# Kernel optimization log

Measured on AMD Instinct MI355X. Metric: run time of the kernel, lower is better.

## Reference

```python
import jax, jax.numpy as jnp
import numpy as np

N_NODES = 100000
N_EDGES = 1600000
D_IN, D_HID, D_OUT = 64, 64, 32


def _glorot(key, shape):
    fan_in, fan_out = shape[0], shape[1]
    lim = np.sqrt(6.0 / (fan_in + fan_out)).astype(np.float32)
    return jax.random.uniform(key, shape, jnp.float32, -lim, lim)


def setup_inputs() -> dict:
    key = jax.random.key(0)
    ks = jax.random.split(key, 12)
    x = jax.random.normal(ks[0], (N_NODES, D_IN), jnp.float32)
    edge_index = jax.random.randint(ks[1], (2, N_EDGES), 0, N_NODES, jnp.int64)
    return {
        "x": x,
        "edge_index": edge_index,
        # SAGEConv 1 (in->hid): lin_l (aggregated neighbors, with bias), lin_r (root, no bias)
        "Wl1": _glorot(ks[2], (D_IN, D_HID)),
        "Wr1": _glorot(ks[3], (D_IN, D_HID)),
        "b1": jnp.zeros((D_HID,), jnp.float32),
        # SAGEConv 2 (hid->out)
        "Wl2": _glorot(ks[4], (D_HID, D_OUT)),
        "Wr2": _glorot(ks[5], (D_HID, D_OUT)),
        "b2": jnp.zeros((D_OUT,), jnp.float32),
        # trust head: Linear(32,16) -> ReLU -> Linear(16,1) -> Sigmoid (dropout inert in eval)
        "Wt1": _glorot(ks[6], (D_OUT, 16)),
        "bt1": jnp.zeros((16,), jnp.float32),
        "Wt2": _glorot(ks[7], (16, 1)),
        "bt2": jnp.zeros((1,), jnp.float32),
    }


def _sage_conv(x, src, dst, Wl, Wr, b):
    # mean-aggregate neighbor messages: msg flows src -> dst
    msg = x[src]                                              # [E, d] gather
    agg_sum = jax.ops.segment_sum(msg, dst, num_segments=N_NODES)
    deg = jax.ops.segment_sum(jnp.ones((src.shape[0],), x.dtype), dst,
                              num_segments=N_NODES)
    agg = agg_sum / jnp.maximum(deg, 1.0)[:, None]            # zero-degree -> 0
    return agg @ Wl + x @ Wr + b


def reference(x, edge_index, Wl1, Wr1, b1, Wl2, Wr2, b2, Wt1, bt1, Wt2, bt2):
    src, dst = edge_index[0], edge_index[1]
    h = _sage_conv(x, src, dst, Wl1, Wr1, b1)
    h = jax.nn.relu(h)                    # dropout p=0.3 inert in eval
    h = _sage_conv(h, src, dst, Wl2, Wr2, b2)
    t = jax.nn.relu(h @ Wt1 + bt1)        # dropout p=0.2 inert in eval
    trust = jax.nn.sigmoid(t @ Wt2 + bt2)
    return h, trust
```

## Files before the change

kernel.cpp:

```cpp
#include <hip/hip_runtime.h>
#include <math.h>


#define NBUCK   1563
#define BCAP    1536
#define BKCHUNK 16384
#define RT      16

typedef __attribute__((ext_vector_type(8))) __bf16 bf16x8;
typedef __attribute__((ext_vector_type(4))) float  f32x4;

union BU { bf16x8 v; unsigned short u[8]; };

__device__ inline unsigned short f2bf(float x) {
    unsigned u = __float_as_uint(x);
    unsigned r = u + 0x7fffu + ((u >> 16) & 1u);
    return (unsigned short)(r >> 16);
}
__device__ inline unsigned pack2(float a, float b) {
    return (unsigned)f2bf(a) | ((unsigned)f2bf(b) << 16);
}
__device__ inline float bflo(unsigned u) { return __uint_as_float(u << 16); }
__device__ inline float bfhi(unsigned u) { return __uint_as_float(u & 0xffff0000u); }
__device__ inline float bf2f(unsigned short h) { return __uint_as_float((unsigned)h << 16); }
__device__ inline unsigned packhl(float x) {
    unsigned short h = f2bf(x);
    unsigned short l = f2bf(x - bf2f(h));
    return (unsigned)h | ((unsigned)l << 16);
}

__global__ __launch_bounds__(256) void k_w(
    const float* __restrict__ Wl1, const float* __restrict__ Wr1,
    const float* __restrict__ Wl2, const float* __restrict__ Wr2,
    unsigned short* __restrict__ Wf)
{
    int tid = threadIdx.x;
    for (int idx = tid; idx < 1536; idx += 256) {
        unsigned short hi8[8], lo8[8];
        int base;
        if (idx < 1024) {
            int q = idx >> 6;
            int l = idx & 63;
            int pass = q >> 3, nf = (q >> 1) & 3, kf = q & 1;
            const float* W = pass ? Wr1 : Wl1;
            int col  = nf * 16 + (l & 15);
            int krow = kf * 32 + (l >> 4) * 8;
            #pragma unroll
            for (int e = 0; e < 8; ++e) {
                float w = W[(krow + e) * 64 + col];
                unsigned short h = f2bf(w);
                hi8[e] = h;
                lo8[e] = f2bf(w - bf2f(h));
            }
            base = (q * 2) * 512 + l * 8;
        } else {
            int i2 = idx - 1024;
            int q2 = i2 >> 6;
            int l = i2 & 63;
            int ntile = q2 >> 1, kf = q2 & 1;
            int col  = ntile * 16 + (l & 15);
            const float* W = (col < 32) ? Wl2 : Wr2;
            int c = col & 31;
            int krow = kf * 32 + (l >> 4) * 8;
            #pragma unroll
            for (int e = 0; e < 8; ++e) {
                float w = W[(krow + e) * 32 + c];
                unsigned short h = f2bf(w);
                hi8[e] = h;
                lo8[e] = f2bf(w - bf2f(h));
            }
            base = (32 + q2 * 2) * 512 + l * 8;
        }
        #pragma unroll
        for (int e = 0; e < 8; ++e) {
            Wf[base + e]       = hi8[e];
            Wf[base + 512 + e] = lo8[e];
        }
    }
}

__global__ __launch_bounds__(256) void k_m1(
    const float* __restrict__ x,
    const unsigned short* __restrict__ Wf, const float* __restrict__ b1,
    unsigned* __restrict__ u16b, float* __restrict__ v,
    const int* __restrict__ src, const int* __restrict__ dst,
    int* __restrict__ gcnt, unsigned* __restrict__ pairs,
    int N, int E, int GB, int BKB)
{
    __shared__ int hist[NBUCK];
    int tid = threadIdx.x;
    int g = blockIdx.x / (RT + 1), r = blockIdx.x % (RT + 1);

    if (r == RT) {
        if (g >= BKB) return;
        int e0 = g * BKCHUNK;
        int e1 = min(e0 + BKCHUNK, E);

        for (int i = tid; i < NBUCK; i += 256) hist[i] = 0;
        __syncthreads();
        for (int e = e0 + tid; e < e1; e += 256)
            atomicAdd(&hist[((unsigned)dst[e]) >> 6], 1);
        __syncthreads();
        int cnt[7], base[7];
        #pragma unroll
        for (int t = 0; t < 7; ++t) {
            int i = tid + t * 256;
            cnt[t] = (i < NBUCK) ? hist[i] : 0;
        }
        #pragma unroll
        for (int t = 0; t < 7; ++t) {
            int i = tid + t * 256;
            base[t] = (i < NBUCK) ? atomicAdd(&gcnt[i], cnt[t]) : 0;
        }
        #pragma unroll
        for (int t = 0; t < 7; ++t) {
            int i = tid + t * 256;
            if (i < NBUCK) hist[i] = i * BCAP + base[t];
        }
        __syncthreads();
        for (int e = e0 + tid; e < e1; e += 256) {
            int t = dst[e];
            int b = ((unsigned)t) >> 6;
            int pos = atomicAdd(&hist[b], 1);
            if (pos < (b + 1) * BCAP)
                pairs[pos] = (unsigned)src[e] | ((unsigned)(t & 63) << 17);
        }
        return;
    }

    int tile = RT * g + r;
    if (tile >= GB) return;
    int nblk = tile * 64;

    int l  = tid & 63, wv = tid >> 6;
    int la = l & 15,   g4 = l >> 4;
    int arow = nblk + wv * 16 + la;
    bool rowOK = (arow < N);

    BU ahi[2], alo[2];
    #pragma unroll
    for (int kf = 0; kf < 2; ++kf) {
        float xv[8];
        if (rowOK) {
            const float* xp = &x[(size_t)arow * 64 + kf * 32 + g4 * 8];
            float4 p0 = *(const float4*)xp;
            float4 p1 = *(const float4*)(xp + 4);
            xv[0] = p0.x; xv[1] = p0.y; xv[2] = p0.z; xv[3] = p0.w;
            xv[4] = p1.x; xv[5] = p1.y; xv[6] = p1.z; xv[7] = p1.w;
        } else {
            #pragma unroll
            for (int e = 0; e < 8; ++e) xv[e] = 0.0f;
        }
        #pragma unroll
        for (int e = 0; e < 8; ++e) {
            unsigned short h = f2bf(xv[e]);
            ahi[kf].u[e] = h;
            alo[kf].u[e] = f2bf(xv[e] - bf2f(h));
        }
    }

    unsigned short* u16 = (unsigned short*)u16b;

    #pragma unroll
    for (int pass = 0; pass < 2; ++pass) {
        #pragma unroll
        for (int nf = 0; nf < 4; ++nf) {
            int n0 = nf * 16;
            f32x4 acc = {0.f, 0.f, 0.f, 0.f};
            #pragma unroll
            for (int kf = 0; kf < 2; ++kf) {
                int q2 = ((pass * 4 + nf) * 2 + kf) * 2;
                bf16x8 bhi = *(const bf16x8*)&Wf[(q2 + 0) * 512 + l * 8];
                bf16x8 blo = *(const bf16x8*)&Wf[(q2 + 1) * 512 + l * 8];
                acc = __builtin_amdgcn_mfma_f32_16x16x32_bf16(ahi[kf].v, bhi, acc, 0, 0, 0);
                acc = __builtin_amdgcn_mfma_f32_16x16x32_bf16(alo[kf].v, bhi, acc, 0, 0, 0);
                acc = __builtin_amdgcn_mfma_f32_16x16x32_bf16(ahi[kf].v, blo, acc, 0, 0, 0);
            }
            if (pass == 0) {
                #pragma unroll
                for (int rr = 0; rr < 4; ++rr) {
                    int nd = nblk + wv * 16 + g4 * 4 + rr;
                    if (nd < N)
                        u16[(size_t)nd * 64 + n0 + la] = f2bf(acc[rr]);
                }
            } else {
                float bb = b1[n0 + la];
                #pragma unroll
                for (int rr = 0; rr < 4; ++rr) {
                    int nd = nblk + wv * 16 + g4 * 4 + rr;
                    if (nd < N)
                        v[(size_t)nd * 64 + n0 + la] = acc[rr] + bb;
                }
            }
        }
    }
}

__global__ __launch_bounds__(512) void k_m2(
    const unsigned* __restrict__ pairs, const int* __restrict__ gcnt,
    const unsigned* __restrict__ u16b, const float* __restrict__ v,
    const unsigned short* __restrict__ Wf, const float* __restrict__ b2,
    unsigned* __restrict__ P16b, float* __restrict__ Qout,
    int2* __restrict__ nodeOff, int* __restrict__ adjG, int N)
{
    __shared__ unsigned sHu[64 * 76];
    __shared__ int   sAdj[BCAP];
    __shared__ int   sOff[65];
    __shared__ int   sCur[64];
    int tid = threadIdx.x;
    int b = blockIdx.x;
    int nodeBase = b * 64;
    int base = b * BCAP;
    int count = min(gcnt[b], BCAP);
    const unsigned* pp = pairs + (size_t)b * BCAP;

    if (tid < 64) sCur[tid] = 0;
    __syncthreads();

    for (int j = tid; j < count; j += 512)
        atomicAdd(&sCur[(pp[j] >> 17) & 63], 1);
    __syncthreads();
    if (tid < 64) {
        int c = sCur[tid];
        int incl = c;
        #pragma unroll
        for (int off = 1; off < 64; off <<= 1) {
            int t = __shfl_up(incl, off);
            if (tid >= off) incl += t;
        }
        sOff[tid] = incl - c;
        if (tid == 63) sOff[64] = incl;
    }
    __syncthreads();
    if (tid < 64) {
        sCur[tid] = sOff[tid];
        int node = nodeBase + tid;
        if (node < N)
            nodeOff[node] = make_int2(base + sOff[tid], sOff[tid + 1] - sOff[tid]);
    }
    __syncthreads();
    for (int j = tid; j < count; j += 512) {
        unsigned e = pp[j];
        int pos = atomicAdd(&sCur[(e >> 17) & 63], 1);
        sAdj[pos] = (int)(e & 0x1FFFFu);
    }
    __syncthreads();
    for (int j = tid; j < count; j += 512) adjG[base + j] = sAdj[j];

    int hw = tid >> 5, lane = tid & 31;
    for (int r = 0; r < 4; ++r) {
        int nl = hw * 4 + r;
        int node = nodeBase + nl;
        float h0 = 0.0f, h1v = 0.0f;
        if (node < N) {
            int beg = sOff[nl], end = sOff[nl + 1];
            float lo[8] = {0,0,0,0,0,0,0,0}, hi[8] = {0,0,0,0,0,0,0,0};
            int i = beg;
            for (; i + 8 <= end; i += 8) {
                int s[8];
                #pragma unroll
                for (int j = 0; j < 8; ++j) s[j] = sAdj[i + j];
                #pragma unroll
                for (int j = 0; j < 8; ++j) {
                    unsigned w = u16b[(size_t)s[j] * 32 + lane];
                    lo[j] += bflo(w); hi[j] += bfhi(w);
                }
            }
            for (; i < end; ++i) {
                unsigned w = u16b[(size_t)sAdj[i] * 32 + lane];
                lo[0] += bflo(w); hi[0] += bfhi(w);
            }
            float mlo = ((lo[0]+lo[1])+(lo[2]+lo[3])) + ((lo[4]+lo[5])+(lo[6]+lo[7]));
            float mhi = ((hi[0]+hi[1])+(hi[2]+hi[3])) + ((hi[4]+hi[5])+(hi[6]+hi[7]));
            int deg = end - beg;
            float invd = (deg > 0) ? 1.0f / (float)deg : 1.0f;
            float2 vv = ((const float2*)v)[(size_t)node * 32 + lane];
            h0  = fmaxf(mlo * invd + vv.x, 0.0f);
            h1v = fmaxf(mhi * invd + vv.y, 0.0f);
        }
        *(uint2*)&sHu[nl * 76 + 2 * lane] = make_uint2(packhl(h0), packhl(h1v));
    }
    __syncthreads();

    int w = tid >> 6, l = tid & 63;
    int la = l & 15, g4 = l >> 4;
    int mtile = w & 3, nt2 = (w >> 2) * 2;

    BU ahi[2], alo[2];
    #pragma unroll
    for (int kf = 0; kf < 2; ++kf) {
        const unsigned* hp = &sHu[(mtile * 16 + la) * 76 + kf * 32 + g4 * 8];
        uint4 a0 = *(const uint4*)hp;
        uint4 a1 = *(const uint4*)(hp + 4);
        unsigned wv8[8] = {a0.x, a0.y, a0.z, a0.w, a1.x, a1.y, a1.z, a1.w};
        #pragma unroll
        for (int e = 0; e < 8; ++e) {
            ahi[kf].u[e] = (unsigned short)wv8[e];
            alo[kf].u[e] = (unsigned short)(wv8[e] >> 16);
        }
    }

    unsigned short* Pus = (unsigned short*)P16b;
    #pragma unroll
    for (int j = 0; j < 2; ++j) {
        int ntile = nt2 + j;
        f32x4 acc = {0.f, 0.f, 0.f, 0.f};
        #pragma unroll
        for (int kf = 0; kf < 2; ++kf) {
            const unsigned short* Wq = Wf + (size_t)(32 + (ntile * 2 + kf) * 2) * 512;
            bf16x8 bhi = *(const bf16x8*)&Wq[l * 8];
            bf16x8 blo = *(const bf16x8*)&Wq[512 + l * 8];
            acc = __builtin_amdgcn_mfma_f32_16x16x32_bf16(ahi[kf].v, bhi, acc, 0, 0, 0);
            acc = __builtin_amdgcn_mfma_f32_16x16x32_bf16(alo[kf].v, bhi, acc, 0, 0, 0);
            acc = __builtin_amdgcn_mfma_f32_16x16x32_bf16(ahi[kf].v, blo, acc, 0, 0, 0);
        }
        int col = ntile * 16 + la;
        if (col < 32) {
            #pragma unroll
            for (int rr = 0; rr < 4; ++rr) {
                int node = nodeBase + mtile * 16 + g4 * 4 + rr;
                if (node < N)
                    Pus[(size_t)node * 32 + col] = f2bf(acc[rr]);
            }
        } else {
            float bb = b2[col - 32];
            #pragma unroll
            for (int rr = 0; rr < 4; ++rr) {
                int node = nodeBase + mtile * 16 + g4 * 4 + rr;
                if (node < N)
                    Qout[(size_t)node * 32 + (col - 32)] = acc[rr] + bb;
            }
        }
    }
}

__global__ __launch_bounds__(256) void k_a2(
    const int2* __restrict__ nodeOff, const int* __restrict__ adj,
    const unsigned* __restrict__ P16b, const float* __restrict__ Q,
    const float* __restrict__ Wt1, const float* __restrict__ bt1,
    const float* __restrict__ Wt2, const float* __restrict__ bt2,
    float* __restrict__ out_h, float* __restrict__ out_trust, int N)
{
    __shared__ float sWt1[32 * 16];
    __shared__ float sWt2[16];
    for (int i = threadIdx.x; i < 512; i += 256) sWt1[i] = Wt1[i];
    if (threadIdx.x < 16) sWt2[threadIdx.x] = Wt2[threadIdx.x];
    __syncthreads();

    int n = blockIdx.x * 16 + (threadIdx.x >> 4);
    int lane = threadIdx.x & 15;
    if (n >= N) return;

    int2 od = nodeOff[n];
    int beg = od.x, end = od.x + od.y;
    float lo[8] = {0,0,0,0,0,0,0,0}, hi[8] = {0,0,0,0,0,0,0,0};
    int i = beg;
    for (; i + 8 <= end; i += 8) {
        int s[8];
        #pragma unroll
        for (int j = 0; j < 8; ++j) s[j] = adj[i + j];
        #pragma unroll
        for (int j = 0; j < 8; ++j) {
            unsigned w = P16b[(size_t)s[j] * 16 + lane];
            lo[j] += bflo(w); hi[j] += bfhi(w);
        }
    }
    for (; i < end; ++i) {
        unsigned w = P16b[(size_t)adj[i] * 16 + lane];
        lo[0] += bflo(w); hi[0] += bfhi(w);
    }
    float invd = (od.y > 0) ? 1.0f / (float)od.y : 1.0f;
    float mlo = (((lo[0]+lo[1])+(lo[2]+lo[3])) + ((lo[4]+lo[5])+(lo[6]+lo[7]))) * invd;
    float mhi = (((hi[0]+hi[1])+(hi[2]+hi[3])) + ((hi[4]+hi[5])+(hi[6]+hi[7]))) * invd;

    float2 qv = ((const float2*)Q)[(size_t)n * 16 + lane];
    float hx = mlo + qv.x;
    float hy = mhi + qv.y;

    ((float2*)out_h)[(size_t)n * 16 + lane] = make_float2(hx, hy);

    float t = bt1[lane];
    #pragma unroll
    for (int k = 0; k < 16; ++k) {
        float hlo = __shfl(hx, k, 16);
        float hhi = __shfl(hy, k, 16);
        t += hlo * sWt1[(2 * k) * 16 + lane] + hhi * sWt1[(2 * k + 1) * 16 + lane];
    }
    t = fmaxf(t, 0.0f);
    float z = t * sWt2[lane];
    z += __shfl_xor(z, 1);
    z += __shfl_xor(z, 2);
    z += __shfl_xor(z, 4);
    z += __shfl_xor(z, 8);
    if (lane == 0) out_trust[n] = 1.0f / (1.0f + expf(-(z + bt2[0])));
}


extern "C" void kernel_launch(void* const* d_in, const int* in_sizes, int n_in,
                              void* d_out, int out_size, void* d_ws, size_t ws_size,
                              hipStream_t stream)
{
    const float* x   = (const float*)d_in[0];
    const int*   ei  = (const int*)d_in[1];
    const float* Wl1 = (const float*)d_in[2];
    const float* Wr1 = (const float*)d_in[3];
    const float* b1  = (const float*)d_in[4];
    const float* Wl2 = (const float*)d_in[5];
    const float* Wr2 = (const float*)d_in[6];
    const float* b2  = (const float*)d_in[7];
    const float* Wt1 = (const float*)d_in[8];
    const float* bt1 = (const float*)d_in[9];
    const float* Wt2 = (const float*)d_in[10];
    const float* bt2 = (const float*)d_in[11];

    const int N = in_sizes[0] / 64;
    const int E = in_sizes[1] / 2;
    const int* src = ei;
    const int* dst = ei + E;

    unsigned* pairs  = (unsigned*)d_ws;
    unsigned* u16b   = pairs + (size_t)NBUCK * BCAP;
    float*    v      = (float*)(u16b + (size_t)N * 32);
    unsigned* P16b   = (unsigned*)(v + (size_t)N * 64);
    float*    Q      = (float*)(P16b + (size_t)N * 16);
    int2*     nodeOff= (int2*)(Q + (size_t)N * 32);
    int*      adj    = (int*)(nodeOff + N);
    int*      gcnt   = adj + (size_t)NBUCK * BCAP;
    unsigned short* Wf = (unsigned short*)(gcnt + 2048);

    hipMemsetAsync(gcnt, 0, 2048 * sizeof(int), stream);

    k_w<<<1, 256, 0, stream>>>(Wl1, Wr1, Wl2, Wr2, Wf);

    const int GB  = (N + 63) / 64;
    const int BKB = (E + BKCHUNK - 1) / BKCHUNK;
    int grp = (GB + RT - 1) / RT > BKB ? (GB + RT - 1) / RT : BKB;
    k_m1<<<(RT + 1) * grp, 256, 0, stream>>>(x, Wf, b1, u16b, v,
                                             src, dst, gcnt, pairs, N, E, GB, BKB);
    k_m2<<<NBUCK, 512, 0, stream>>>(pairs, gcnt, u16b, v, Wf, b2,
                                    P16b, Q, nodeOff, adj, N);

    float* out_h     = (float*)d_out;
    float* out_trust = out_h + (size_t)N * 32;
    k_a2<<<(N + 15) / 16, 256, 0, stream>>>(nodeOff, adj, P16b, Q,
                                            Wt1, bt1, Wt2, bt2,
                                            out_h, out_trust, N);
}
```

Before: 249.9 us.

## Rebalance edge-bucketing blocks and widen layer-2 neighbor gather to 16-byte loads

Layer-1 tiles are now interleaved with edge-bucketing blocks at a 4:1 ratio instead of 16:1, and each bucketing block handles 4096 edges instead of 16384, so the histogram work is spread across more blocks that run alongside the GEMM tiles. In k_m2 the mean-aggregation now gives each wave 8 nodes, with 8 lanes per neighbor row loading 16 bytes each and 8 neighbors processed in parallel. Partial sums are combined with cross-lane shuffles. This is meant to raise memory-level parallelism in the gather, at the cost of shuffle reductions, extra global atomics on gcnt, and idle lanes on low-degree nodes.

```diff
diff --git a/kernel.cpp b/kernel.cpp
--- a/kernel.cpp
+++ b/kernel.cpp
@@ -4,8 +4,7 @@
 
 #define NBUCK   1563
 #define BCAP    1536
-#define BKCHUNK 16384
-#define RT      16
+#define BKCHUNK 4096
 
 typedef __attribute__((ext_vector_type(8))) __bf16 bf16x8;
 typedef __attribute__((ext_vector_type(4))) float  f32x4;
@@ -16,9 +15,6 @@
     unsigned u = __float_as_uint(x);
     unsigned r = u + 0x7fffu + ((u >> 16) & 1u);
     return (unsigned short)(r >> 16);
-}
-__device__ inline unsigned pack2(float a, float b) {
-    return (unsigned)f2bf(a) | ((unsigned)f2bf(b) << 16);
 }
 __device__ inline float bflo(unsigned u) { return __uint_as_float(u << 16); }
 __device__ inline float bfhi(unsigned u) { return __uint_as_float(u & 0xffff0000u); }
@@ -89,9 +85,9 @@
 {
     __shared__ int hist[NBUCK];
     int tid = threadIdx.x;
-    int g = blockIdx.x / (RT + 1), r = blockIdx.x % (RT + 1);
-
-    if (r == RT) {
+    int g = blockIdx.x / 5, r5 = blockIdx.x % 5;
+
+    if (r5 == 4) {
         if (g >= BKB) return;
         int e0 = g * BKCHUNK;
         int e1 = min(e0 + BKCHUNK, E);
@@ -128,7 +124,7 @@
         return;
     }
 
-    int tile = RT * g + r;
+    int tile = 4 * g + r5;
     if (tile >= GB) return;
     int nblk = tile * 64;
 
@@ -247,42 +243,81 @@
     __syncthreads();
     for (int j = tid; j < count; j += 512) adjG[base + j] = sAdj[j];
 
-    int hw = tid >> 5, lane = tid & 31;
-    for (int r = 0; r < 4; ++r) {
-        int nl = hw * 4 + r;
+    int w = tid >> 6, ln = tid & 63;
+    int q = ln >> 3, f8 = ln & 7;
+    for (int r = 0; r < 8; ++r) {
+        int nl = w * 8 + r;
         int node = nodeBase + nl;
-        float h0 = 0.0f, h1v = 0.0f;
-        if (node < N) {
-            int beg = sOff[nl], end = sOff[nl + 1];
-            float lo[8] = {0,0,0,0,0,0,0,0}, hi[8] = {0,0,0,0,0,0,0,0};
-            int i = beg;
-            for (; i + 8 <= end; i += 8) {
-                int s[8];
+        int beg = sOff[nl], end = sOff[nl + 1];
+        float a0[8] = {0,0,0,0,0,0,0,0}, a1[8] = {0,0,0,0,0,0,0,0};
+        int i = beg;
+        for (; i + 16 <= end; i += 16) {
+            int s0 = sAdj[i + q];
+            int s1 = sAdj[i + 8 + q];
+            uint4 w0 = *(const uint4*)&u16b[(size_t)s0 * 32 + f8 * 4];
+            uint4 w1 = *(const uint4*)&u16b[(size_t)s1 * 32 + f8 * 4];
+            a0[0] += bflo(w0.x); a0[1] += bfhi(w0.x);
+            a0[2] += bflo(w0.y); a0[3] += bfhi(w0.y);
+            a0[4] += bflo(w0.z); a0[5] += bfhi(w0.z);
+            a0[6] += bflo(w0.w); a0[7] += bfhi(w0.w);
+            a1[0] += bflo(w1.x); a1[1] += bfhi(w1.x);
+            a1[2] += bflo(w1.y); a1[3] += bfhi(w1.y);
+            a1[4] += bflo(w1.z); a1[5] += bfhi(w1.z);
+            a1[6] += bflo(w1.w); a1[7] += bfhi(w1.w);
+        }
+        {
+            int i0 = i + q, i1 = i + 8 + q;
+            if (i0 < end) {
+                uint4 w0 = *(const uint4*)&u16b[(size_t)sAdj[i0] * 32 + f8 * 4];
+                a0[0] += bflo(w0.x); a0[1] += bfhi(w0.x);
+                a0[2] += bflo(w0.y); a0[3] += bfhi(w0.y);
+                a0[4] += bflo(w0.z); a0[5] += bfhi(w0.z);
+                a0[6] += bflo(w0.w); a0[7] += bfhi(w0.w);
+            }
+            if (i1 < end) {
+                uint4 w1 = *(const uint4*)&u16b[(size_t)sAdj[i1] * 32 + f8 * 4];
+                a1[0] += bflo(w1.x); a1[1] += bfhi(w1.x);
+                a1[2] += bflo(w1.y); a1[3] += bfhi(w1.y);
+                a1[4] += bflo(w1.z); a1[5] += bfhi(w1.z);
+                a1[6] += bflo(w1.w); a1[7] += bfhi(w1.w);
+            }
+        }
+        #pragma unroll
+        for (int e = 0; e < 8; ++e) {
+            float s = a0[e] + a1[e];
+            s += __shfl_xor(s, 8);
+            s += __shfl_xor(s, 16);
+            s += __shfl_xor(s, 32);
+            a0[e] = s;
+        }
+        if (q == 0) {
+            float h[8];
+            if (node < N) {
+                int deg = end - beg;
+                float invd = (deg > 0) ? 1.0f / (float)deg : 1.0f;
+                float4 v0 = *(const float4*)&v[(size_t)node * 64 + f8 * 8];
+                float4 v1 = *(const float4*)&v[(size_t)node * 64 + f8 * 8 + 4];
+                h[0] = fmaxf(a0[0] * invd + v0.x, 0.0f);
+                h[1] = fmaxf(a0[1] * invd + v0.y, 0.0f);
+                h[2] = fmaxf(a0[2] * invd + v0.z, 0.0f);
+                h[3] = fmaxf(a0[3] * invd + v0.w, 0.0f);
+                h[4] = fmaxf(a0[4] * invd + v1.x, 0.0f);
+                h[5] = fmaxf(a0[5] * invd + v1.y, 0.0f);
+                h[6] = fmaxf(a0[6] * invd + v1.z, 0.0f);
+                h[7] = fmaxf(a0[7] * invd + v1.w, 0.0f);
+            } else {
                 #pragma unroll
-                for (int j = 0; j < 8; ++j) s[j] = sAdj[i + j];
-                #pragma unroll
-                for (int j = 0; j < 8; ++j) {
-                    unsigned w = u16b[(size_t)s[j] * 32 + lane];
-                    lo[j] += bflo(w); hi[j] += bfhi(w);
-                }
-            }
-            for (; i < end; ++i) {
-                unsigned w = u16b[(size_t)sAdj[i] * 32 + lane];
-                lo[0] += bflo(w); hi[0] += bfhi(w);
-            }
-            float mlo = ((lo[0]+lo[1])+(lo[2]+lo[3])) + ((lo[4]+lo[5])+(lo[6]+lo[7]));
-            float mhi = ((hi[0]+hi[1])+(hi[2]+hi[3])) + ((hi[4]+hi[5])+(hi[6]+hi[7]));
-            int deg = end - beg;
-            float invd = (deg > 0) ? 1.0f / (float)deg : 1.0f;
-            float2 vv = ((const float2*)v)[(size_t)node * 32 + lane];
-            h0  = fmaxf(mlo * invd + vv.x, 0.0f);
-            h1v = fmaxf(mhi * invd + vv.y, 0.0f);
-        }
-        *(uint2*)&sHu[nl * 76 + 2 * lane] = make_uint2(packhl(h0), packhl(h1v));
-    }
-    __syncthreads();
-
-    int w = tid >> 6, l = tid & 63;
+                for (int e = 0; e < 8; ++e) h[e] = 0.0f;
+            }
+            uint4 o0 = make_uint4(packhl(h[0]), packhl(h[1]), packhl(h[2]), packhl(h[3]));
+            uint4 o1 = make_uint4(packhl(h[4]), packhl(h[5]), packhl(h[6]), packhl(h[7]));
+            *(uint4*)&sHu[nl * 76 + f8 * 8]     = o0;
+            *(uint4*)&sHu[nl * 76 + f8 * 8 + 4] = o1;
+        }
+    }
+    __syncthreads();
+
+    int l = tid & 63;
     int la = l & 15, g4 = l >> 4;
     int mtile = w & 3, nt2 = (w >> 2) * 2;
 
@@ -434,9 +469,9 @@
 
     const int GB  = (N + 63) / 64;
     const int BKB = (E + BKCHUNK - 1) / BKCHUNK;
-    int grp = (GB + RT - 1) / RT > BKB ? (GB + RT - 1) / RT : BKB;
-    k_m1<<<(RT + 1) * grp, 256, 0, stream>>>(x, Wf, b1, u16b, v,
-                                             src, dst, gcnt, pairs, N, E, GB, BKB);
+    int grp = (GB + 3) / 4 > BKB ? (GB + 3) / 4 : BKB;
+    k_m1<<<5 * grp, 256, 0, stream>>>(x, Wf, b1, u16b, v,
+                                      src, dst, gcnt, pairs, N, E, GB, BKB);
     k_m2<<<NBUCK, 512, 0, stream>>>(pairs, gcnt, u16b, v, Wf, b2,
                                     P16b, Q, nodeOff, adj, N);
 
```

New measurement: 235.9 us. 1.06x faster.
